# Kernel tuning notes

Measured on AMD Instinct MI355X. Metric: run time of the kernel, lower is better.

The kernel has to match this reference:

```python
import jax, jax.numpy as jnp
import numpy as np

B, M, D = 8192, 64, 256
NEG = -1e9  # masking value for invalid (padded) memory slots


def setup_inputs() -> dict:
    key = jax.random.key(0)
    ks = jax.random.split(key, 8)
    s = 1.0 / np.sqrt(D)  # nn.Linear default init scale
    return {
        "h_tilde": jax.random.normal(ks[0], (B, D), jnp.float32),
        "mem": jax.random.normal(ks[1], (B, M, D), jnp.float32),
        "lengths": jax.random.randint(ks[2], (B,), 0, M + 1, jnp.int32),
        "Wg_w": jax.random.uniform(ks[3], (D, D), jnp.float32, -s, s),
        "Wg_b": jax.random.uniform(ks[4], (D,), jnp.float32, -s, s),
        "Ug_w": jax.random.uniform(ks[5], (D, D), jnp.float32, -s, s),
        "Ug_b": jax.random.uniform(ks[6], (D,), jnp.float32, -s, s),
        "b_g": jnp.zeros((D,), jnp.float32),
    }


def reference(h_tilde, mem, lengths, Wg_w, Wg_b, Ug_w, Ug_b, b_g):
    # valid-slot mask: [B, M]
    valid = jnp.arange(M)[None, :] < lengths[:, None]
    # per-sample attention over ragged memory
    scores = jnp.einsum("bmd,bd->bm", mem, h_tilde)          # [B, M]
    attn = jax.nn.softmax(jnp.where(valid, scores, NEG), axis=1)
    r = jnp.einsum("bm,bmd->bd", attn, mem)                   # [B, D]
    # gated fusion (two Linears + extra bias)
    g = jax.nn.sigmoid(h_tilde @ Wg_w.T + Wg_b + r @ Ug_w.T + Ug_b + b_g)
    fused = g * r + (1.0 - g) * h_tilde
    # empty-memory samples pass through h_tilde unchanged
    has_mem = (lengths > 0)[:, None]
    return jnp.where(has_mem, fused, h_tilde)
```

## Files before the change

kernel.cpp:

```cpp
#include <hip/hip_runtime.h>
#include <hip/hip_bf16.h>

#define BB 8192
#define MM 64
#define DD 256
#define NEGV -1e9f
#define PSTR 68

typedef __attribute__((ext_vector_type(8))) short frag_ab;
typedef __attribute__((ext_vector_type(4))) float f32x4;

__device__ inline short f2bs(float f) {
    __hip_bfloat16 v = __float2bfloat16(f);
    return *reinterpret_cast<short*>(&v);
}
__device__ inline float blo(unsigned w) { return __uint_as_float(w << 16); }
__device__ inline float bhi(unsigned w) { return __uint_as_float(w & 0xffff0000u); }

__global__ __launch_bounds__(256, 6) void attn_kernel(
    const float* __restrict__ h, const float* __restrict__ mem,
    const int* __restrict__ len, float* __restrict__ r_out)
{
    __shared__ float part[MM * PSTR];
    __shared__ float score_s[MM];
    __shared__ __align__(16) float attn_s[MM];
    __shared__ __align__(16) float rpart[4 * DD];

    const int b    = blockIdx.x;
    const int t    = threadIdx.x;
    const int lane = t & 63;
    const int wave = t >> 6;
    const int L    = len[b];
    const int nrows = min(16, max(0, L - wave * 16));

    const float4 hv = *reinterpret_cast<const float4*>(h + (size_t)b * DD + 4 * lane);
    const float* mbase = mem + (size_t)b * MM * DD + (size_t)(wave * 16) * DD + 4 * lane;

    unsigned tile[32];
    float p[16];
    #pragma unroll
    for (int i = 0; i < 16; ++i) { tile[2 * i] = 0u; tile[2 * i + 1] = 0u; p[i] = 0.f; }
    #pragma unroll
    for (int i = 0; i < 16; ++i) {
        if (i < nrows) {
            const float4 v = *reinterpret_cast<const float4*>(mbase + i * DD);
            p[i] = v.x * hv.x + v.y * hv.y + v.z * hv.z + v.w * hv.w;
            __hip_bfloat162 q0 = __float22bfloat162_rn(float2{v.x, v.y});
            __hip_bfloat162 q1 = __float22bfloat162_rn(float2{v.z, v.w});
            tile[2 * i]     = *reinterpret_cast<unsigned*>(&q0);
            tile[2 * i + 1] = *reinterpret_cast<unsigned*>(&q1);
        }
    }
    #pragma unroll
    for (int i = 0; i < 16; ++i)
        part[(wave * 16 + i) * PSTR + lane] = p[i];
    __syncthreads();

    {
        const int m = t >> 2, c = t & 3;
        const float4* pr = reinterpret_cast<const float4*>(part + m * PSTR + c * 16);
        const float4 s0 = pr[0], s1 = pr[1], s2 = pr[2], s3 = pr[3];
        float s = (s0.x + s0.y + s0.z + s0.w) + (s1.x + s1.y + s1.z + s1.w)
                + (s2.x + s2.y + s2.z + s2.w) + (s3.x + s3.y + s3.z + s3.w);
        s += __shfl_xor(s, 1, 64);
        s += __shfl_xor(s, 2, 64);
        if (c == 0) score_s[m] = (m < L) ? s : NEGV;
    }
    __syncthreads();

    if (t < 64) {
        const float s = score_s[t];
        float mx = s;
        #pragma unroll
        for (int off = 32; off > 0; off >>= 1)
            mx = fmaxf(mx, __shfl_xor(mx, off, 64));
        const float e = __expf(s - mx);
        float den = e;
        #pragma unroll
        for (int off = 32; off > 0; off >>= 1)
            den += __shfl_xor(den, off, 64);
        attn_s[t] = e / den;
    }
    __syncthreads();

    float4 rp = {0.f, 0.f, 0.f, 0.f};
    if (nrows > 0) {
        #pragma unroll
        for (int ic = 0; ic < 4; ++ic) {
            const float4 aw = *reinterpret_cast<const float4*>(attn_s + wave * 16 + 4 * ic);
            const float a[4] = {aw.x, aw.y, aw.z, aw.w};
            #pragma unroll
            for (int k = 0; k < 4; ++k) {
                const int i = 4 * ic + k;
                rp.x += a[k] * blo(tile[2 * i]);
                rp.y += a[k] * bhi(tile[2 * i]);
                rp.z += a[k] * blo(tile[2 * i + 1]);
                rp.w += a[k] * bhi(tile[2 * i + 1]);
            }
        }
    }
    *reinterpret_cast<float4*>(rpart + wave * DD + 4 * lane) = rp;
    __syncthreads();

    const float r = rpart[t] + rpart[DD + t] + rpart[2 * DD + t] + rpart[3 * DD + t];
    r_out[(size_t)b * DD + t] = r;
}

__global__ __launch_bounds__(256) void gate_kernel(
    const float* __restrict__ h, const float* __restrict__ r,
    const int* __restrict__ len,
    const float* __restrict__ Wg_w, const float* __restrict__ Wg_b,
    const float* __restrict__ Ug_w, const float* __restrict__ Ug_b,
    const float* __restrict__ b_g, float* __restrict__ out)
{
    __shared__ __hip_bfloat16 Ah[64 * 32];
    __shared__ __hip_bfloat16 Ar[64 * 32];
    __shared__ __hip_bfloat16 Wgs[64 * 32];
    __shared__ __hip_bfloat16 Wus[64 * 32];

    const int t    = threadIdx.x;
    const int lane = t & 63;
    const int wave = t >> 6;
    const int brow0 = blockIdx.x * 64;
    const int dcol0 = blockIdx.y * 64;

    const int srow = t >> 2;
    const int skq  = t & 3;

    const f32x4 zero = {0.f, 0.f, 0.f, 0.f};
    f32x4 acc[4];
    #pragma unroll
    for (int ct = 0; ct < 4; ++ct) acc[ct] = zero;

    const int arow_m = (lane & 15);
    const int kchunk = (lane >> 4) * 8;

    const float* hp = h    + (size_t)(brow0 + srow) * DD + skq * 8;
    const float* rp = r    + (size_t)(brow0 + srow) * DD + skq * 8;
    const float* gp = Wg_w + (size_t)(dcol0 + srow) * DD + skq * 8;
    const float* up = Ug_w + (size_t)(dcol0 + srow) * DD + skq * 8;

    for (int k0 = 0; k0 < DD; k0 += 32) {
        const float4 h0 = *reinterpret_cast<const float4*>(hp + k0);
        const float4 h1 = *reinterpret_cast<const float4*>(hp + k0 + 4);
        const float4 r0 = *reinterpret_cast<const float4*>(rp + k0);
        const float4 r1 = *reinterpret_cast<const float4*>(rp + k0 + 4);
        const float4 g0 = *reinterpret_cast<const float4*>(gp + k0);
        const float4 g1 = *reinterpret_cast<const float4*>(gp + k0 + 4);
        const float4 u0 = *reinterpret_cast<const float4*>(up + k0);
        const float4 u1 = *reinterpret_cast<const float4*>(up + k0 + 4);

        __syncthreads();
        frag_ab fh, fr, fg, fu;
        fh[0]=f2bs(h0.x); fh[1]=f2bs(h0.y); fh[2]=f2bs(h0.z); fh[3]=f2bs(h0.w);
        fh[4]=f2bs(h1.x); fh[5]=f2bs(h1.y); fh[6]=f2bs(h1.z); fh[7]=f2bs(h1.w);
        fr[0]=f2bs(r0.x); fr[1]=f2bs(r0.y); fr[2]=f2bs(r0.z); fr[3]=f2bs(r0.w);
        fr[4]=f2bs(r1.x); fr[5]=f2bs(r1.y); fr[6]=f2bs(r1.z); fr[7]=f2bs(r1.w);
        fg[0]=f2bs(g0.x); fg[1]=f2bs(g0.y); fg[2]=f2bs(g0.z); fg[3]=f2bs(g0.w);
        fg[4]=f2bs(g1.x); fg[5]=f2bs(g1.y); fg[6]=f2bs(g1.z); fg[7]=f2bs(g1.w);
        fu[0]=f2bs(u0.x); fu[1]=f2bs(u0.y); fu[2]=f2bs(u0.z); fu[3]=f2bs(u0.w);
        fu[4]=f2bs(u1.x); fu[5]=f2bs(u1.y); fu[6]=f2bs(u1.z); fu[7]=f2bs(u1.w);
        *reinterpret_cast<frag_ab*>(&Ah [srow * 32 + skq * 8]) = fh;
        *reinterpret_cast<frag_ab*>(&Ar [srow * 32 + skq * 8]) = fr;
        *reinterpret_cast<frag_ab*>(&Wgs[srow * 32 + skq * 8]) = fg;
        *reinterpret_cast<frag_ab*>(&Wus[srow * 32 + skq * 8]) = fu;
        __syncthreads();

        const frag_ab afh = *reinterpret_cast<const frag_ab*>(
            &Ah[(wave * 16 + arow_m) * 32 + kchunk]);
        const frag_ab afr = *reinterpret_cast<const frag_ab*>(
            &Ar[(wave * 16 + arow_m) * 32 + kchunk]);
        #pragma unroll
        for (int ct = 0; ct < 4; ++ct) {
            const frag_ab wfg = *reinterpret_cast<const frag_ab*>(
                &Wgs[(ct * 16 + arow_m) * 32 + kchunk]);
            const frag_ab wfu = *reinterpret_cast<const frag_ab*>(
                &Wus[(ct * 16 + arow_m) * 32 + kchunk]);
            acc[ct] = __builtin_amdgcn_mfma_f32_16x16x32_bf16(afh, wfg, acc[ct], 0, 0, 0);
            acc[ct] = __builtin_amdgcn_mfma_f32_16x16x32_bf16(afr, wfu, acc[ct], 0, 0, 0);
        }
    }

    float bias_v[4];
    #pragma unroll
    for (int ct = 0; ct < 4; ++ct) {
        const int d = dcol0 + ct * 16 + (lane & 15);
        bias_v[ct] = Wg_b[d] + Ug_b[d] + b_g[d];
    }
    const int rbase = brow0 + wave * 16 + (lane >> 4) * 4;
    #pragma unroll
    for (int i = 0; i < 4; ++i) {
        const int bb = rbase + i;
        const int lb = len[bb];
        #pragma unroll
        for (int ct = 0; ct < 4; ++ct) {
            const int d = dcol0 + ct * 16 + (lane & 15);
            const float x = acc[ct][i] + bias_v[ct];
            const float g = 1.f / (1.f + __expf(-x));
            const size_t idx = (size_t)bb * DD + d;
            const float rv = r[idx];
            const float hvv = h[idx];
            out[idx] = (lb > 0) ? (hvv + g * (rv - hvv)) : hvv;
        }
    }
}

extern "C" void kernel_launch(void* const* d_in, const int* in_sizes, int n_in,
                              void* d_out, int out_size, void* d_ws, size_t ws_size,
                              hipStream_t stream) {
    const float* h    = (const float*)d_in[0];
    const float* mem  = (const float*)d_in[1];
    const int*   len  = (const int*)d_in[2];
    const float* Wg_w = (const float*)d_in[3];
    const float* Wg_b = (const float*)d_in[4];
    const float* Ug_w = (const float*)d_in[5];
    const float* Ug_b = (const float*)d_in[6];
    const float* b_g  = (const float*)d_in[7];
    float* out  = (float*)d_out;
    float* r_ws = (float*)d_ws;

    attn_kernel<<<BB, 256, 0, stream>>>(h, mem, len, r_ws);
    gate_kernel<<<dim3(BB / 64, DD / 64), 256, 0, stream>>>(
        h, r_ws, len, Wg_w, Wg_b, Ug_w, Ug_b, b_g, out);
}
```

Measured before the change: 690.2 us.

## Keep fp32 memory tile in registers and load MFMA fragments directly from global

The attention kernel now keeps the loaded memory rows as fp32 float4 registers instead of packing them to bf16. This drops the conversion work and improves the precision of r, but doubles the register footprint, so the occupancy hint drops from 6 to 4 blocks. The gate kernel removes its shared-memory staging and barriers: each lane loads its MFMA fragments directly from global memory, converts them to bf16 and fully unrolls the K loop. Weight rows are now re-read from global or cache by every wave instead of being shared through LDS.

```diff
diff --git a/kernel.cpp b/kernel.cpp
--- a/kernel.cpp
+++ b/kernel.cpp
@@ -14,10 +14,15 @@
     __hip_bfloat16 v = __float2bfloat16(f);
     return *reinterpret_cast<short*>(&v);
 }
-__device__ inline float blo(unsigned w) { return __uint_as_float(w << 16); }
-__device__ inline float bhi(unsigned w) { return __uint_as_float(w & 0xffff0000u); }
 
-__global__ __launch_bounds__(256, 6) void attn_kernel(
+__device__ inline frag_ab pack8(const float4 a, const float4 b) {
+    frag_ab f;
+    f[0] = f2bs(a.x); f[1] = f2bs(a.y); f[2] = f2bs(a.z); f[3] = f2bs(a.w);
+    f[4] = f2bs(b.x); f[5] = f2bs(b.y); f[6] = f2bs(b.z); f[7] = f2bs(b.w);
+    return f;
+}
+
+__global__ __launch_bounds__(256, 4) void attn_kernel(
     const float* __restrict__ h, const float* __restrict__ mem,
     const int* __restrict__ len, float* __restrict__ r_out)
 {
@@ -36,24 +41,18 @@
     const float4 hv = *reinterpret_cast<const float4*>(h + (size_t)b * DD + 4 * lane);
     const float* mbase = mem + (size_t)b * MM * DD + (size_t)(wave * 16) * DD + 4 * lane;
 
-    unsigned tile[32];
-    float p[16];
+    float4 v[16];
     #pragma unroll
-    for (int i = 0; i < 16; ++i) { tile[2 * i] = 0u; tile[2 * i + 1] = 0u; p[i] = 0.f; }
+    for (int i = 0; i < 16; ++i) v[i] = float4{0.f, 0.f, 0.f, 0.f};
     #pragma unroll
     for (int i = 0; i < 16; ++i) {
-        if (i < nrows) {
-            const float4 v = *reinterpret_cast<const float4*>(mbase + i * DD);
-            p[i] = v.x * hv.x + v.y * hv.y + v.z * hv.z + v.w * hv.w;
-            __hip_bfloat162 q0 = __float22bfloat162_rn(float2{v.x, v.y});
-            __hip_bfloat162 q1 = __float22bfloat162_rn(float2{v.z, v.w});
-            tile[2 * i]     = *reinterpret_cast<unsigned*>(&q0);
-            tile[2 * i + 1] = *reinterpret_cast<unsigned*>(&q1);
-        }
+        if (i < nrows)
+            v[i] = *reinterpret_cast<const float4*>(mbase + i * DD);
     }
     #pragma unroll
     for (int i = 0; i < 16; ++i)
-        part[(wave * 16 + i) * PSTR + lane] = p[i];
+        part[(wave * 16 + i) * PSTR + lane] =
+            v[i].x * hv.x + v[i].y * hv.y + v[i].z * hv.z + v[i].w * hv.w;
     __syncthreads();
 
     {
@@ -92,10 +91,10 @@
             #pragma unroll
             for (int k = 0; k < 4; ++k) {
                 const int i = 4 * ic + k;
-                rp.x += a[k] * blo(tile[2 * i]);
-                rp.y += a[k] * bhi(tile[2 * i]);
-                rp.z += a[k] * blo(tile[2 * i + 1]);
-                rp.w += a[k] * bhi(tile[2 * i + 1]);
+                rp.x += a[k] * v[i].x;
+                rp.y += a[k] * v[i].y;
+                rp.z += a[k] * v[i].z;
+                rp.w += a[k] * v[i].w;
             }
         }
     }
@@ -106,76 +105,48 @@
     r_out[(size_t)b * DD + t] = r;
 }
 
-__global__ __launch_bounds__(256) void gate_kernel(
+__global__ __launch_bounds__(256, 2) void gate_kernel(
     const float* __restrict__ h, const float* __restrict__ r,
     const int* __restrict__ len,
     const float* __restrict__ Wg_w, const float* __restrict__ Wg_b,
     const float* __restrict__ Ug_w, const float* __restrict__ Ug_b,
     const float* __restrict__ b_g, float* __restrict__ out)
 {
-    __shared__ __hip_bfloat16 Ah[64 * 32];
-    __shared__ __hip_bfloat16 Ar[64 * 32];
-    __shared__ __hip_bfloat16 Wgs[64 * 32];
-    __shared__ __hip_bfloat16 Wus[64 * 32];
-
     const int t    = threadIdx.x;
     const int lane = t & 63;
     const int wave = t >> 6;
     const int brow0 = blockIdx.x * 64;
     const int dcol0 = blockIdx.y * 64;
 
-    const int srow = t >> 2;
-    const int skq  = t & 3;
+    const int am = lane & 15;
+    const int kc = (lane >> 4) * 8;
+
+    const float* hp = h + (size_t)(brow0 + wave * 16 + am) * DD + kc;
+    const float* rp = r + (size_t)(brow0 + wave * 16 + am) * DD + kc;
+    const float* gp = Wg_w + (size_t)(dcol0 + am) * DD + kc;
+    const float* up = Ug_w + (size_t)(dcol0 + am) * DD + kc;
 
     const f32x4 zero = {0.f, 0.f, 0.f, 0.f};
     f32x4 acc[4];
     #pragma unroll
     for (int ct = 0; ct < 4; ++ct) acc[ct] = zero;
 
-    const int arow_m = (lane & 15);
-    const int kchunk = (lane >> 4) * 8;
-
-    const float* hp = h    + (size_t)(brow0 + srow) * DD + skq * 8;
-    const float* rp = r    + (size_t)(brow0 + srow) * DD + skq * 8;
-    const float* gp = Wg_w + (size_t)(dcol0 + srow) * DD + skq * 8;
-    const float* up = Ug_w + (size_t)(dcol0 + srow) * DD + skq * 8;
-
+    #pragma unroll
     for (int k0 = 0; k0 < DD; k0 += 32) {
         const float4 h0 = *reinterpret_cast<const float4*>(hp + k0);
         const float4 h1 = *reinterpret_cast<const float4*>(hp + k0 + 4);
         const float4 r0 = *reinterpret_cast<const float4*>(rp + k0);
         const float4 r1 = *reinterpret_cast<const float4*>(rp + k0 + 4);
-        const float4 g0 = *reinterpret_cast<const float4*>(gp + k0);
-        const float4 g1 = *reinterpret_cast<const float4*>(gp + k0 + 4);
-        const float4 u0 = *reinterpret_cast<const float4*>(up + k0);
-        const float4 u1 = *reinterpret_cast<const float4*>(up + k0 + 4);
-
-        __syncthreads();
-        frag_ab fh, fr, fg, fu;
-        fh[0]=f2bs(h0.x); fh[1]=f2bs(h0.y); fh[2]=f2bs(h0.z); fh[3]=f2bs(h0.w);
-        fh[4]=f2bs(h1.x); fh[5]=f2bs(h1.y); fh[6]=f2bs(h1.z); fh[7]=f2bs(h1.w);
-        fr[0]=f2bs(r0.x); fr[1]=f2bs(r0.y); fr[2]=f2bs(r0.z); fr[3]=f2bs(r0.w);
-        fr[4]=f2bs(r1.x); fr[5]=f2bs(r1.y); fr[6]=f2bs(r1.z); fr[7]=f2bs(r1.w);
-        fg[0]=f2bs(g0.x); fg[1]=f2bs(g0.y); fg[2]=f2bs(g0.z); fg[3]=f2bs(g0.w);
-        fg[4]=f2bs(g1.x); fg[5]=f2bs(g1.y); fg[6]=f2bs(g1.z); fg[7]=f2bs(g1.w);
-        fu[0]=f2bs(u0.x); fu[1]=f2bs(u0.y); fu[2]=f2bs(u0.z); fu[3]=f2bs(u0.w);
-        fu[4]=f2bs(u1.x); fu[5]=f2bs(u1.y); fu[6]=f2bs(u1.z); fu[7]=f2bs(u1.w);
-        *reinterpret_cast<frag_ab*>(&Ah [srow * 32 + skq * 8]) = fh;
-        *reinterpret_cast<frag_ab*>(&Ar [srow * 32 + skq * 8]) = fr;
-        *reinterpret_cast<frag_ab*>(&Wgs[srow * 32 + skq * 8]) = fg;
-        *reinterpret_cast<frag_ab*>(&Wus[srow * 32 + skq * 8]) = fu;
-        __syncthreads();
-
-        const frag_ab afh = *reinterpret_cast<const frag_ab*>(
-            &Ah[(wave * 16 + arow_m) * 32 + kchunk]);
-        const frag_ab afr = *reinterpret_cast<const frag_ab*>(
-            &Ar[(wave * 16 + arow_m) * 32 + kchunk]);
+        const frag_ab afh = pack8(h0, h1);
+        const frag_ab afr = pack8(r0, r1);
         #pragma unroll
         for (int ct = 0; ct < 4; ++ct) {
-            const frag_ab wfg = *reinterpret_cast<const frag_ab*>(
-                &Wgs[(ct * 16 + arow_m) * 32 + kchunk]);
-            const frag_ab wfu = *reinterpret_cast<const frag_ab*>(
-                &Wus[(ct * 16 + arow_m) * 32 + kchunk]);
+            const float4 g0 = *reinterpret_cast<const float4*>(gp + (size_t)ct * 16 * DD + k0);
+            const float4 g1 = *reinterpret_cast<const float4*>(gp + (size_t)ct * 16 * DD + k0 + 4);
+            const float4 u0 = *reinterpret_cast<const float4*>(up + (size_t)ct * 16 * DD + k0);
+            const float4 u1 = *reinterpret_cast<const float4*>(up + (size_t)ct * 16 * DD + k0 + 4);
+            const frag_ab wfg = pack8(g0, g1);
+            const frag_ab wfu = pack8(u0, u1);
             acc[ct] = __builtin_amdgcn_mfma_f32_16x16x32_bf16(afh, wfg, acc[ct], 0, 0, 0);
             acc[ct] = __builtin_amdgcn_mfma_f32_16x16x32_bf16(afr, wfu, acc[ct], 0, 0, 0);
         }
@@ -184,7 +155,7 @@
     float bias_v[4];
     #pragma unroll
     for (int ct = 0; ct < 4; ++ct) {
-        const int d = dcol0 + ct * 16 + (lane & 15);
+        const int d = dcol0 + ct * 16 + am;
         bias_v[ct] = Wg_b[d] + Ug_b[d] + b_g[d];
     }
     const int rbase = brow0 + wave * 16 + (lane >> 4) * 4;
@@ -194,7 +165,7 @@
         const int lb = len[bb];
         #pragma unroll
         for (int ct = 0; ct < 4; ++ct) {
-            const int d = dcol0 + ct * 16 + (lane & 15);
+            const int d = dcol0 + ct * 16 + am;
             const float x = acc[ct][i] + bias_v[ct];
             const float g = 1.f / (1.f + __expf(-x));
             const size_t idx = (size_t)bb * DD + d;
```

After: 696.6 us. No clear change (+0.9%).
